# Kernel tuning notes

Hardware: AMD Instinct MI355X
Metric: run time of the kernel (lower is better)

## Reference

```python
import jax, jax.numpy as jnp
import numpy as np

NUM_NODES = 10000
NUM_EDGES = 640000
IN_CH = 128
HID = 128
OUT_CH = 1


def setup_inputs() -> dict:
    key = jax.random.key(0)
    ks = jax.random.split(key, 12)
    x = jax.random.normal(ks[0], (NUM_NODES, IN_CH), dtype=jnp.float32)
    edge_index = jax.random.randint(ks[1], (2, NUM_EDGES), 0, NUM_NODES, dtype=jnp.int64)
    edge_weight = jax.random.uniform(ks[2], (NUM_EDGES,), dtype=jnp.float32)
    s1 = 1.0 / np.sqrt(IN_CH)
    s2 = 1.0 / np.sqrt(HID)
    W1 = jax.random.uniform(ks[3], (HID, IN_CH), minval=-s1, maxval=s1, dtype=jnp.float32)
    b1 = jnp.zeros((HID,), dtype=jnp.float32)
    W2 = jax.random.uniform(ks[4], (HID, HID), minval=-s2, maxval=s2, dtype=jnp.float32)
    b2 = jnp.zeros((HID,), dtype=jnp.float32)
    sc = 1.0 / np.sqrt(HID * 3)
    conv_w = jax.random.uniform(ks[5], (HID, HID, 3), minval=-sc, maxval=sc, dtype=jnp.float32)
    conv_b = jax.random.uniform(ks[6], (HID,), minval=-sc, maxval=sc, dtype=jnp.float32)
    fc_w = jax.random.uniform(ks[7], (OUT_CH, HID), minval=-s2, maxval=s2, dtype=jnp.float32)
    fc_b = jax.random.uniform(ks[8], (OUT_CH,), minval=-s2, maxval=s2, dtype=jnp.float32)
    return {"x": x, "edge_index": edge_index, "edge_weight": edge_weight,
            "W1": W1, "b1": b1, "W2": W2, "b2": b2,
            "conv_w": conv_w, "conv_b": conv_b, "fc_w": fc_w, "fc_b": fc_b}


def _gcn_conv(x, row, col, norm, W, b):
    # PyG GCNConv: linear (no bias in lin), normalized scatter-add, then bias
    xw = x @ W.T                                   # [N, out]
    msg = xw[row] * norm[:, None]                  # gather + edge scale [E, out]
    out = jax.ops.segment_sum(msg, col, num_segments=NUM_NODES)
    return out + b


def reference(x, edge_index, edge_weight, W1, b1, W2, b2, conv_w, conv_b, fc_w, fc_b):
    # gcn_norm with self-loops (fill_value=1.0)
    loop = jnp.arange(NUM_NODES, dtype=edge_index.dtype)
    row = jnp.concatenate([edge_index[0], loop])
    col = jnp.concatenate([edge_index[1], loop])
    w = jnp.concatenate([edge_weight, jnp.ones((NUM_NODES,), dtype=edge_weight.dtype)])
    deg = jax.ops.segment_sum(w, col, num_segments=NUM_NODES)
    dinv = jnp.where(deg > 0, jax.lax.rsqrt(deg), 0.0)
    norm = dinv[row] * w * dinv[col]

    h = jax.nn.relu(_gcn_conv(x, row, col, norm, W1, b1))
    # dropout is identity in eval mode
    h = jax.nn.relu(_gcn_conv(h, row, col, norm, W2, b2))

    # temporal conv1d over node axis: [N,H] -> [1,H,N]
    hc = h.T[None, :, :]
    hc = jax.lax.conv_general_dilated(hc, conv_w, window_strides=(1,),
                                      padding='SAME',
                                      dimension_numbers=('NCH', 'OIH', 'NCH'))
    hc = hc + conv_b[None, :, None]
    h = hc[0].T                                    # [N, H]

    return (h @ fc_w.T + fc_b).squeeze()           # [N]
```

## Files before the change

### kernel.cpp

```cpp
#include <hip/hip_runtime.h>

#define N_NODES 10000
#define N_EDGES 640000
#define CH 128
#define NHB 128
#define EPB (N_EDGES / NHB)
#define NCHUNK 40

__global__ __launch_bounds__(256) void hist_kernel(const int* __restrict__ ei,
                                                   const float* __restrict__ ew,
                                                   int* __restrict__ hist,
                                                   float* __restrict__ dhist) {
    __shared__ int h[N_NODES];
    __shared__ float hf[N_NODES];
    int b = blockIdx.x, t = threadIdx.x;
    for (int i = t; i < N_NODES; i += 256) { h[i] = 0; hf[i] = 0.0f; }
    __syncthreads();
    int e0 = b * EPB;
    for (int i = t; i < EPB; i += 256) {
        int c = ei[N_EDGES + e0 + i];
        float w = ew[e0 + i];
        atomicAdd(&h[c], 1);
        atomicAdd(&hf[c], w);
    }
    __syncthreads();
    for (int i = t; i < N_NODES; i += 256) {
        hist[b * N_NODES + i] = h[i];
        dhist[b * N_NODES + i] = hf[i];
    }
}

__global__ __launch_bounds__(256) void reduce_kernel(const int* __restrict__ hist,
        const float* __restrict__ dhist, int* __restrict__ tot,
        float* __restrict__ dinv,
        const float* __restrict__ conv_w, const float* __restrict__ conv_b,
        const float* __restrict__ fc_w, const float* __restrict__ fc_b,
        float* __restrict__ vbuf, float* __restrict__ c0) {
    int blk = blockIdx.x, t = threadIdx.x;
    if (blk == NCHUNK) {
        for (int i = t; i <= 384; i += 256) {
            if (i < 384) {
                float s = 0.0f;
                for (int o = 0; o < CH; ++o) s += fc_w[o] * conv_w[o * 384 + i];
                vbuf[i] = s;
            } else {
                float s = fc_b[0];
                for (int o = 0; o < CH; ++o) s += fc_w[o] * conv_b[o];
                *c0 = s;
            }
        }
        return;
    }
    int n = blk * 256 + t;
    if (n >= N_NODES) return;
    int c = 0; float d = 0.0f;
    #pragma unroll 4
    for (int b = 0; b < NHB; ++b) {
        c += hist[b * N_NODES + n];
        d += dhist[b * N_NODES + n];
    }
    tot[n] = c;
    dinv[n] = rsqrtf(d + 1.0f);
}

__global__ __launch_bounds__(256) void bofs_kernel(int* __restrict__ hist,
        const int* __restrict__ tot, int* __restrict__ offs) {
    __shared__ int wred[4];
    __shared__ int wsum[4];
    __shared__ int base_s;
    int blk = blockIdx.x, t = threadIdx.x;
    int lane = t & 63, wave = t >> 6;
    int partial = 0;
    int lim = blk * 256;
    for (int i = t; i < lim; i += 256) partial += tot[i];
    int s = partial;
    #pragma unroll
    for (int off = 32; off > 0; off >>= 1) s += __shfl_down(s, off, 64);
    if (lane == 0) wred[wave] = s;
    __syncthreads();
    if (t == 0) base_s = wred[0] + wred[1] + wred[2] + wred[3];
    __syncthreads();
    int base = base_s;
    int n = blk * 256 + t;
    int v = (n < N_NODES) ? tot[n] : 0;
    s = v;
    #pragma unroll
    for (int off = 1; off < 64; off <<= 1) {
        int u = __shfl_up(s, off, 64);
        if (lane >= off) s += u;
    }
    if (lane == 63) wsum[wave] = s;
    __syncthreads();
    int wbase = 0;
    for (int i = 0; i < wave; ++i) wbase += wsum[i];
    if (n < N_NODES) {
        int run = base + wbase + s - v;
        offs[n] = run;
        for (int b = 0; b < NHB; ++b) {
            int hh = hist[b * N_NODES + n];
            hist[b * N_NODES + n] = run;
            run += hh;
        }
    }
}

__global__ __launch_bounds__(256) void scatter_kernel(const int* __restrict__ ei,
        const float* __restrict__ ew, const float* __restrict__ dinv,
        const int* __restrict__ bofs, int2* __restrict__ erec) {
    __shared__ int cur[N_NODES];
    __shared__ float di[N_NODES];
    int b = blockIdx.x, t = threadIdx.x;
    for (int i = t; i < N_NODES; i += 256) {
        cur[i] = bofs[b * N_NODES + i];
        di[i] = dinv[i];
    }
    __syncthreads();
    int e0 = b * EPB;
    for (int i = t; i < EPB; i += 256) {
        int e = e0 + i;
        int r = ei[e];
        int c = ei[N_EDGES + e];
        int p = atomicAdd(&cur[c], 1);
        float v = di[r] * ew[e] * di[c];
        erec[p] = make_int2(r, __float_as_int(v));
    }
}

__global__ __launch_bounds__(256) void gemm128_kernel(const float* __restrict__ A,
                                                      const float* __restrict__ W,
                                                      float* __restrict__ out, int M) {
    __shared__ float As[32][68];
    __shared__ float Ws[32][132];
    int tid = threadIdx.x;
    int tx = tid & 31;
    int ty = tid >> 5;
    int row0 = blockIdx.x * 64;
    float acc[8][4] = {};
    for (int k0 = 0; k0 < 128; k0 += 32) {
        #pragma unroll
        for (int i = 0; i < 8; ++i) {
            int idx = tid + i * 256;
            int r = idx >> 5, k = idx & 31;
            int gr = row0 + r;
            As[k][r] = (gr < M) ? A[gr * CH + k0 + k] : 0.0f;
        }
        #pragma unroll
        for (int i = 0; i < 16; ++i) {
            int idx = tid + i * 256;
            int o = idx >> 5, k = idx & 31;
            Ws[k][o] = W[o * CH + k0 + k];
        }
        __syncthreads();
        #pragma unroll
        for (int kk = 0; kk < 32; ++kk) {
            float a[8], w[4];
            #pragma unroll
            for (int j = 0; j < 8; ++j) a[j] = As[kk][ty * 8 + j];
            #pragma unroll
            for (int c = 0; c < 4; ++c) w[c] = Ws[kk][tx * 4 + c];
            #pragma unroll
            for (int j = 0; j < 8; ++j)
                #pragma unroll
                for (int c = 0; c < 4; ++c)
                    acc[j][c] += a[j] * w[c];
        }
        __syncthreads();
    }
    #pragma unroll
    for (int j = 0; j < 8; ++j) {
        int gr = row0 + ty * 8 + j;
        if (gr < M) {
            float4 v = make_float4(acc[j][0], acc[j][1], acc[j][2], acc[j][3]);
            *reinterpret_cast<float4*>(&out[gr * CH + tx * 4]) = v;
        }
    }
}

__global__ __launch_bounds__(256) void agg_kernel(const float4* __restrict__ xw4,
        const int2* __restrict__ erec, const int* __restrict__ offs,
        const int* __restrict__ cnt, const float* __restrict__ dinv,
        const float4* __restrict__ bias4, float4* __restrict__ out4) {
    int l = threadIdx.x & 31;
    int g = threadIdx.x >> 5;
    int n = blockIdx.x * 8 + g;
    float d = dinv[n];
    float dd = d * d;
    float4 self = xw4[n * 32 + l];
    float4 acc = make_float4(dd * self.x, dd * self.y, dd * self.z, dd * self.w);
    int start = offs[n];
    int num = cnt[n];
    int i = 0;
    for (; i + 8 <= num; i += 8) {
        int2 r[8];
        #pragma unroll
        for (int j = 0; j < 8; ++j) r[j] = erec[start + i + j];
        float4 f[8];
        #pragma unroll
        for (int j = 0; j < 8; ++j) f[j] = xw4[r[j].x * 32 + l];
        #pragma unroll
        for (int j = 0; j < 8; ++j) {
            float v = __int_as_float(r[j].y);
            acc.x += v * f[j].x; acc.y += v * f[j].y;
            acc.z += v * f[j].z; acc.w += v * f[j].w;
        }
    }
    for (; i < num; ++i) {
        int2 r = erec[start + i];
        float4 f = xw4[r.x * 32 + l];
        float v = __int_as_float(r.y);
        acc.x += v * f.x; acc.y += v * f.y; acc.z += v * f.z; acc.w += v * f.w;
    }
    float4 bb = bias4[l];
    acc.x = fmaxf(acc.x + bb.x, 0.0f);
    acc.y = fmaxf(acc.y + bb.y, 0.0f);
    acc.z = fmaxf(acc.z + bb.z, 0.0f);
    acc.w = fmaxf(acc.w + bb.w, 0.0f);
    out4[n * 32 + l] = acc;
}

__global__ __launch_bounds__(256) void convfc_kernel(const float4* __restrict__ h4,
        const float* __restrict__ vbuf, const float* __restrict__ c0,
        float* __restrict__ out) {
    int l = threadIdx.x & 31;
    int g = threadIdx.x >> 5;
    int n = blockIdx.x * 8 + g;
    float v00 = vbuf[(4 * l + 0) * 3 + 0], v01 = vbuf[(4 * l + 0) * 3 + 1], v02 = vbuf[(4 * l + 0) * 3 + 2];
    float v10 = vbuf[(4 * l + 1) * 3 + 0], v11 = vbuf[(4 * l + 1) * 3 + 1], v12 = vbuf[(4 * l + 1) * 3 + 2];
    float v20 = vbuf[(4 * l + 2) * 3 + 0], v21 = vbuf[(4 * l + 2) * 3 + 1], v22 = vbuf[(4 * l + 2) * 3 + 2];
    float v30 = vbuf[(4 * l + 3) * 3 + 0], v31 = vbuf[(4 * l + 3) * 3 + 1], v32 = vbuf[(4 * l + 3) * 3 + 2];
    float4 hm = h4[n * 32 + l];
    float p = hm.x * v01 + hm.y * v11 + hm.z * v21 + hm.w * v31;
    if (n > 0) {
        float4 ha = h4[(n - 1) * 32 + l];
        p += ha.x * v00 + ha.y * v10 + ha.z * v20 + ha.w * v30;
    }
    if (n < N_NODES - 1) {
        float4 hb = h4[(n + 1) * 32 + l];
        p += hb.x * v02 + hb.y * v12 + hb.z * v22 + hb.w * v32;
    }
    #pragma unroll
    for (int off = 16; off > 0; off >>= 1) p += __shfl_down(p, off, 32);
    if (l == 0) out[n] = p + *c0;
}

extern "C" void kernel_launch(void* const* d_in, const int* in_sizes, int n_in,
                              void* d_out, int out_size, void* d_ws, size_t ws_size,
                              hipStream_t stream) {
    const float* x       = (const float*)d_in[0];
    const int*   ei      = (const int*)d_in[1];
    const float* ew      = (const float*)d_in[2];
    const float* W1      = (const float*)d_in[3];
    const float* b1      = (const float*)d_in[4];
    const float* W2      = (const float*)d_in[5];
    const float* b2      = (const float*)d_in[6];
    const float* conv_w  = (const float*)d_in[7];
    const float* conv_b  = (const float*)d_in[8];
    const float* fc_w    = (const float*)d_in[9];
    const float* fc_b    = (const float*)d_in[10];
    float* out = (float*)d_out;

    float* bufA   = (float*)d_ws;
    float* bufB   = bufA + N_NODES * CH;
    int2*  erec   = (int2*)(bufB + N_NODES * CH);
    int*   hist   = (int*)bufA;
    float* dhist  = (float*)erec;
    int*   tot    = (int*)(erec + N_EDGES);
    int*   offs   = tot + N_NODES;
    float* dinv   = (float*)(offs + N_NODES);
    float* vbuf   = dinv + N_NODES;
    float* c0     = vbuf + 384;

    hist_kernel<<<NHB, 256, 0, stream>>>(ei, ew, hist, dhist);
    reduce_kernel<<<NCHUNK + 1, 256, 0, stream>>>(hist, dhist, tot, dinv,
                                                  conv_w, conv_b, fc_w, fc_b, vbuf, c0);
    bofs_kernel<<<NCHUNK, 256, 0, stream>>>(hist, tot, offs);
    scatter_kernel<<<NHB, 256, 0, stream>>>(ei, ew, dinv, hist, erec);

    const int gemm_grid = (N_NODES + 63) / 64;
    gemm128_kernel<<<gemm_grid, 256, 0, stream>>>(x, W1, bufA, N_NODES);
    agg_kernel<<<N_NODES / 8, 256, 0, stream>>>((const float4*)bufA, erec, offs, tot,
                                                dinv, (const float4*)b1, (float4*)bufB);
    gemm128_kernel<<<gemm_grid, 256, 0, stream>>>(bufB, W2, bufA, N_NODES);
    agg_kernel<<<N_NODES / 8, 256, 0, stream>>>((const float4*)bufA, erec, offs, tot,
                                                dinv, (const float4*)b2, (float4*)bufB);
    convfc_kernel<<<N_NODES / 8, 256, 0, stream>>>((const float4*)bufB, vbuf, c0, out);
}
```

Measured before the change: 236.4 us.

## Fuse histogram, first GEMM and weight-folding into one launch; merge reduce with block offsets

The per-block edge histogram, the first node-feature GEMM and the conv/fc weight folding now run as different block roles inside a single kernel, sharing one shared-memory union. The histogram blocks also write per-chunk partial sums, so the degree reduction and the prefix-offset computation can merge into one kernel. This cuts two launches and lets the independent GEMM overlap with the histogram work. In exchange it uses separate workspace buffers for hist/dhist and xw1/xw2, a larger workspace footprint, and a heavier shared-memory allocation for the fused blocks.

```diff
diff --git a/kernel.cpp b/kernel.cpp
--- a/kernel.cpp
+++ b/kernel.cpp
@@ -6,135 +6,15 @@
 #define NHB 128
 #define EPB (N_EDGES / NHB)
 #define NCHUNK 40
-
-__global__ __launch_bounds__(256) void hist_kernel(const int* __restrict__ ei,
-                                                   const float* __restrict__ ew,
-                                                   int* __restrict__ hist,
-                                                   float* __restrict__ dhist) {
-    __shared__ int h[N_NODES];
-    __shared__ float hf[N_NODES];
-    int b = blockIdx.x, t = threadIdx.x;
-    for (int i = t; i < N_NODES; i += 256) { h[i] = 0; hf[i] = 0.0f; }
-    __syncthreads();
-    int e0 = b * EPB;
-    for (int i = t; i < EPB; i += 256) {
-        int c = ei[N_EDGES + e0 + i];
-        float w = ew[e0 + i];
-        atomicAdd(&h[c], 1);
-        atomicAdd(&hf[c], w);
-    }
-    __syncthreads();
-    for (int i = t; i < N_NODES; i += 256) {
-        hist[b * N_NODES + i] = h[i];
-        dhist[b * N_NODES + i] = hf[i];
-    }
-}
-
-__global__ __launch_bounds__(256) void reduce_kernel(const int* __restrict__ hist,
-        const float* __restrict__ dhist, int* __restrict__ tot,
-        float* __restrict__ dinv,
-        const float* __restrict__ conv_w, const float* __restrict__ conv_b,
-        const float* __restrict__ fc_w, const float* __restrict__ fc_b,
-        float* __restrict__ vbuf, float* __restrict__ c0) {
-    int blk = blockIdx.x, t = threadIdx.x;
-    if (blk == NCHUNK) {
-        for (int i = t; i <= 384; i += 256) {
-            if (i < 384) {
-                float s = 0.0f;
-                for (int o = 0; o < CH; ++o) s += fc_w[o] * conv_w[o * 384 + i];
-                vbuf[i] = s;
-            } else {
-                float s = fc_b[0];
-                for (int o = 0; o < CH; ++o) s += fc_w[o] * conv_b[o];
-                *c0 = s;
-            }
-        }
-        return;
-    }
-    int n = blk * 256 + t;
-    if (n >= N_NODES) return;
-    int c = 0; float d = 0.0f;
-    #pragma unroll 4
-    for (int b = 0; b < NHB; ++b) {
-        c += hist[b * N_NODES + n];
-        d += dhist[b * N_NODES + n];
-    }
-    tot[n] = c;
-    dinv[n] = rsqrtf(d + 1.0f);
-}
-
-__global__ __launch_bounds__(256) void bofs_kernel(int* __restrict__ hist,
-        const int* __restrict__ tot, int* __restrict__ offs) {
-    __shared__ int wred[4];
-    __shared__ int wsum[4];
-    __shared__ int base_s;
-    int blk = blockIdx.x, t = threadIdx.x;
-    int lane = t & 63, wave = t >> 6;
-    int partial = 0;
-    int lim = blk * 256;
-    for (int i = t; i < lim; i += 256) partial += tot[i];
-    int s = partial;
-    #pragma unroll
-    for (int off = 32; off > 0; off >>= 1) s += __shfl_down(s, off, 64);
-    if (lane == 0) wred[wave] = s;
-    __syncthreads();
-    if (t == 0) base_s = wred[0] + wred[1] + wred[2] + wred[3];
-    __syncthreads();
-    int base = base_s;
-    int n = blk * 256 + t;
-    int v = (n < N_NODES) ? tot[n] : 0;
-    s = v;
-    #pragma unroll
-    for (int off = 1; off < 64; off <<= 1) {
-        int u = __shfl_up(s, off, 64);
-        if (lane >= off) s += u;
-    }
-    if (lane == 63) wsum[wave] = s;
-    __syncthreads();
-    int wbase = 0;
-    for (int i = 0; i < wave; ++i) wbase += wsum[i];
-    if (n < N_NODES) {
-        int run = base + wbase + s - v;
-        offs[n] = run;
-        for (int b = 0; b < NHB; ++b) {
-            int hh = hist[b * N_NODES + n];
-            hist[b * N_NODES + n] = run;
-            run += hh;
-        }
-    }
-}
-
-__global__ __launch_bounds__(256) void scatter_kernel(const int* __restrict__ ei,
-        const float* __restrict__ ew, const float* __restrict__ dinv,
-        const int* __restrict__ bofs, int2* __restrict__ erec) {
-    __shared__ int cur[N_NODES];
-    __shared__ float di[N_NODES];
-    int b = blockIdx.x, t = threadIdx.x;
-    for (int i = t; i < N_NODES; i += 256) {
-        cur[i] = bofs[b * N_NODES + i];
-        di[i] = dinv[i];
-    }
-    __syncthreads();
-    int e0 = b * EPB;
-    for (int i = t; i < EPB; i += 256) {
-        int e = e0 + i;
-        int r = ei[e];
-        int c = ei[N_EDGES + e];
-        int p = atomicAdd(&cur[c], 1);
-        float v = di[r] * ew[e] * di[c];
-        erec[p] = make_int2(r, __float_as_int(v));
-    }
-}
-
-__global__ __launch_bounds__(256) void gemm128_kernel(const float* __restrict__ A,
-                                                      const float* __restrict__ W,
-                                                      float* __restrict__ out, int M) {
-    __shared__ float As[32][68];
-    __shared__ float Ws[32][132];
+#define GT 157
+
+__device__ __forceinline__ void gemm_tile(const float* __restrict__ A,
+        const float* __restrict__ W, float* __restrict__ out, int tile,
+        float (*As)[68], float (*Ws)[132]) {
     int tid = threadIdx.x;
     int tx = tid & 31;
     int ty = tid >> 5;
-    int row0 = blockIdx.x * 64;
+    int row0 = tile * 64;
     float acc[8][4] = {};
     for (int k0 = 0; k0 < 128; k0 += 32) {
         #pragma unroll
@@ -142,7 +22,7 @@
             int idx = tid + i * 256;
             int r = idx >> 5, k = idx & 31;
             int gr = row0 + r;
-            As[k][r] = (gr < M) ? A[gr * CH + k0 + k] : 0.0f;
+            As[k][r] = (gr < N_NODES) ? A[gr * CH + k0 + k] : 0.0f;
         }
         #pragma unroll
         for (int i = 0; i < 16; ++i) {
@@ -169,11 +49,154 @@
     #pragma unroll
     for (int j = 0; j < 8; ++j) {
         int gr = row0 + ty * 8 + j;
-        if (gr < M) {
+        if (gr < N_NODES) {
             float4 v = make_float4(acc[j][0], acc[j][1], acc[j][2], acc[j][3]);
             *reinterpret_cast<float4*>(&out[gr * CH + tx * 4]) = v;
         }
     }
+}
+
+__global__ __launch_bounds__(256) void build1_kernel(
+        const float* __restrict__ x, const int* __restrict__ ei,
+        const float* __restrict__ ew, const float* __restrict__ W1,
+        const float* __restrict__ conv_w, const float* __restrict__ conv_b,
+        const float* __restrict__ fc_w, const float* __restrict__ fc_b,
+        float* __restrict__ xw1, int* __restrict__ hist, float* __restrict__ dhist,
+        int* __restrict__ chunk_sum, float* __restrict__ vbuf, float* __restrict__ c0) {
+    __shared__ union {
+        struct { int h[N_NODES]; float hf[N_NODES]; } hist;
+        struct { float As[32][68]; float Ws[32][132]; } gemm;
+    } sm;
+    __shared__ int wred[4];
+    const int b = blockIdx.x, t = threadIdx.x;
+
+    if (b < NHB) {
+        for (int i = t; i < N_NODES; i += 256) { sm.hist.h[i] = 0; sm.hist.hf[i] = 0.0f; }
+        __syncthreads();
+        int e0 = b * EPB;
+        for (int i = t; i < EPB; i += 256) {
+            int c = ei[N_EDGES + e0 + i];
+            float w = ew[e0 + i];
+            atomicAdd(&sm.hist.h[c], 1);
+            atomicAdd(&sm.hist.hf[c], w);
+        }
+        __syncthreads();
+        int lane = t & 63, wave = t >> 6;
+        for (int j = 0; j < NCHUNK; ++j) {
+            int i = j * 256 + t;
+            int val = 0;
+            if (i < N_NODES) {
+                val = sm.hist.h[i];
+                hist[b * N_NODES + i] = val;
+                dhist[b * N_NODES + i] = sm.hist.hf[i];
+            }
+            int s = val;
+            #pragma unroll
+            for (int off = 32; off > 0; off >>= 1) s += __shfl_down(s, off, 64);
+            if (lane == 0) wred[wave] = s;
+            __syncthreads();
+            if (t == 0) chunk_sum[j * NHB + b] = wred[0] + wred[1] + wred[2] + wred[3];
+            __syncthreads();
+        }
+    } else if (b < NHB + GT) {
+        gemm_tile(x, W1, xw1, b - NHB, sm.gemm.As, sm.gemm.Ws);
+    } else {
+        for (int i = t; i <= 384; i += 256) {
+            if (i < 384) {
+                float s = 0.0f;
+                for (int o = 0; o < CH; ++o) s += fc_w[o] * conv_w[o * 384 + i];
+                vbuf[i] = s;
+            } else {
+                float s = fc_b[0];
+                for (int o = 0; o < CH; ++o) s += fc_w[o] * conv_b[o];
+                *c0 = s;
+            }
+        }
+    }
+}
+
+__global__ __launch_bounds__(256) void reducebofs_kernel(int* __restrict__ hist,
+        const float* __restrict__ dhist, const int* __restrict__ chunk_sum,
+        int* __restrict__ tot, int* __restrict__ offs, float* __restrict__ dinv) {
+    __shared__ int wred[4];
+    __shared__ int wsum[4];
+    __shared__ int base_s;
+    const int blk = blockIdx.x, t = threadIdx.x;
+    const int lane = t & 63, wave = t >> 6;
+
+    int part = 0;
+    for (int idx = t; idx < NCHUNK * NHB; idx += 256) {
+        int j = idx >> 7;
+        if (j < blk) part += chunk_sum[idx];
+    }
+    int s = part;
+    #pragma unroll
+    for (int off = 32; off > 0; off >>= 1) s += __shfl_down(s, off, 64);
+    if (lane == 0) wred[wave] = s;
+    __syncthreads();
+    if (t == 0) base_s = wred[0] + wred[1] + wred[2] + wred[3];
+
+    int n = blk * 256 + t;
+    int c = 0;
+    if (n < N_NODES) {
+        float d = 0.0f;
+        #pragma unroll 4
+        for (int bb = 0; bb < NHB; ++bb) {
+            c += hist[bb * N_NODES + n];
+            d += dhist[bb * N_NODES + n];
+        }
+        tot[n] = c;
+        dinv[n] = rsqrtf(d + 1.0f);
+    }
+    s = c;
+    #pragma unroll
+    for (int off = 1; off < 64; off <<= 1) {
+        int u = __shfl_up(s, off, 64);
+        if (lane >= off) s += u;
+    }
+    if (lane == 63) wsum[wave] = s;
+    __syncthreads();
+    int wbase = 0;
+    for (int i = 0; i < wave; ++i) wbase += wsum[i];
+    if (n < N_NODES) {
+        int run = base_s + wbase + s - c;
+        offs[n] = run;
+        for (int bb = 0; bb < NHB; ++bb) {
+            int hh = hist[bb * N_NODES + n];
+            hist[bb * N_NODES + n] = run;
+            run += hh;
+        }
+    }
+}
+
+__global__ __launch_bounds__(256) void scatter_kernel(const int* __restrict__ ei,
+        const float* __restrict__ ew, const float* __restrict__ dinv,
+        const int* __restrict__ bofs, int2* __restrict__ erec) {
+    __shared__ int cur[N_NODES];
+    __shared__ float di[N_NODES];
+    int b = blockIdx.x, t = threadIdx.x;
+    for (int i = t; i < N_NODES; i += 256) {
+        cur[i] = bofs[b * N_NODES + i];
+        di[i] = dinv[i];
+    }
+    __syncthreads();
+    int e0 = b * EPB;
+    for (int i = t; i < EPB; i += 256) {
+        int e = e0 + i;
+        int r = ei[e];
+        int c = ei[N_EDGES + e];
+        int p = atomicAdd(&cur[c], 1);
+        float v = di[r] * ew[e] * di[c];
+        erec[p] = make_int2(r, __float_as_int(v));
+    }
+}
+
+__global__ __launch_bounds__(256) void gemm128_kernel(const float* __restrict__ A,
+                                                      const float* __restrict__ W,
+                                                      float* __restrict__ out) {
+    __shared__ float As[32][68];
+    __shared__ float Ws[32][132];
+    gemm_tile(A, W, out, blockIdx.x, As, Ws);
 }
 
 __global__ __launch_bounds__(256) void agg_kernel(const float4* __restrict__ xw4,
@@ -259,29 +282,28 @@
     const float* fc_b    = (const float*)d_in[10];
     float* out = (float*)d_out;
 
-    float* bufA   = (float*)d_ws;
-    float* bufB   = bufA + N_NODES * CH;
-    int2*  erec   = (int2*)(bufB + N_NODES * CH);
-    int*   hist   = (int*)bufA;
-    float* dhist  = (float*)erec;
-    int*   tot    = (int*)(erec + N_EDGES);
+    float* xw1    = (float*)d_ws;
+    float* bufB   = xw1 + N_NODES * CH;
+    float* xw2    = bufB + N_NODES * CH;
+    int2*  erec   = (int2*)(xw2 + N_NODES * CH);
+    int*   hist   = (int*)(erec + N_EDGES);
+    float* dhist  = (float*)(hist + NHB * N_NODES);
+    int*   chunks = (int*)(dhist + NHB * N_NODES);
+    int*   tot    = chunks + NCHUNK * NHB;
     int*   offs   = tot + N_NODES;
     float* dinv   = (float*)(offs + N_NODES);
     float* vbuf   = dinv + N_NODES;
     float* c0     = vbuf + 384;
 
-    hist_kernel<<<NHB, 256, 0, stream>>>(ei, ew, hist, dhist);
-    reduce_kernel<<<NCHUNK + 1, 256, 0, stream>>>(hist, dhist, tot, dinv,
-                                                  conv_w, conv_b, fc_w, fc_b, vbuf, c0);
-    bofs_kernel<<<NCHUNK, 256, 0, stream>>>(hist, tot, offs);
+    build1_kernel<<<NHB + GT + 1, 256, 0, stream>>>(x, ei, ew, W1, conv_w, conv_b,
+                                                    fc_w, fc_b, xw1, hist, dhist,
+                                                    chunks, vbuf, c0);
+    reducebofs_kernel<<<NCHUNK, 256, 0, stream>>>(hist, dhist, chunks, tot, offs, dinv);
     scatter_kernel<<<NHB, 256, 0, stream>>>(ei, ew, dinv, hist, erec);
-
-    const int gemm_grid = (N_NODES + 63) / 64;
-    gemm128_kernel<<<gemm_grid, 256, 0, stream>>>(x, W1, bufA, N_NODES);
-    agg_kernel<<<N_NODES / 8, 256, 0, stream>>>((const float4*)bufA, erec, offs, tot,
+    agg_kernel<<<N_NODES / 8, 256, 0, stream>>>((const float4*)xw1, erec, offs, tot,
                                                 dinv, (const float4*)b1, (float4*)bufB);
-    gemm128_kernel<<<gemm_grid, 256, 0, stream>>>(bufB, W2, bufA, N_NODES);
-    agg_kernel<<<N_NODES / 8, 256, 0, stream>>>((const float4*)bufA, erec, offs, tot,
+    gemm128_kernel<<<GT, 256, 0, stream>>>(bufB, W2, xw2);
+    agg_kernel<<<N_NODES / 8, 256, 0, stream>>>((const float4*)xw2, erec, offs, tot,
                                                 dinv, (const float4*)b2, (float4*)bufB);
     convfc_kernel<<<N_NODES / 8, 256, 0, stream>>>((const float4*)bufB, vbuf, c0, out);
 }
```

Result: slower. 244.1 us (+3.3%).
